# Performance work log

Hardware: AMD Instinct MI355X
Metric: run time of the kernel (lower is better)

Reference implementation:

```python
import jax, jax.numpy as jnp
import numpy as np

# irreps layout: 256x0e (dim 256) + 128x1o (dim 384) + 64x2e (dim 320) -> total 960
MULS = (256, 128, 64)
DIMS = (1, 3, 5)  # 2l+1 for l = 0, 1, 2


def setup_inputs() -> dict:
    key = jax.random.key(0)
    k0, k1, k2, k3 = jax.random.split(key, 4)
    N = 131072
    total = sum(m * d for m, d in zip(MULS, DIMS))  # 960
    return {
        "features": jax.random.normal(k0, (N, total), dtype=jnp.float32),
        "w0": jax.random.normal(k1, (256, 256), dtype=jnp.float32),
        "w1": jax.random.normal(k2, (128, 128), dtype=jnp.float32),
        "w2": jax.random.normal(k3, (64, 64), dtype=jnp.float32),
    }


def _linear_irreps(features, weights):
    # Equivariant Linear == block-diagonal per-irrep matmul over the multiplicity
    # axis, broadcast over the (2l+1) m-components, scaled by 1/sqrt(mul_in)
    # (the net of e3nn's path_weight sqrt((2l+1)/mul_in) and the w3j 1/sqrt(2l+1)).
    outs = []
    off = 0
    for w, mul, d in zip(weights, MULS, DIMS):
        x = features[:, off:off + mul * d].reshape(-1, mul, d)  # [N, u, i]
        scale = 1.0 / np.sqrt(mul).astype(np.float32)
        y = jnp.einsum('zui,uw->zwi', x, w) * scale  # [N, w, i]
        outs.append(y.reshape(y.shape[0], mul * d))
        off += mul * d
    return jnp.concatenate(outs, axis=-1)  # [N, 960]


def reference(features, w0, w1, w2):
    return _linear_irreps(features, (w0, w1, w2))
```

## Files before the change

kernel.cpp:

```cpp
#include <hip/hip_runtime.h>
#include <hip/hip_bf16.h>

typedef short bf16x8 __attribute__((ext_vector_type(8)));
typedef float f32x4 __attribute__((ext_vector_type(4)));
typedef unsigned short u16t;

__device__ __forceinline__ u16t f2bf(float f) {
    return __builtin_bit_cast(u16t, __float2bfloat16(f));
}

__device__ __forceinline__ f32x4 mfma16(bf16x8 a, bf16x8 b, f32x4 c) {
    return __builtin_amdgcn_mfma_f32_16x16x32_bf16(a, b, c, 0, 0, 0);
}

template<int D, int MUL>
__global__ void expand_w(const float* __restrict__ w, u16t* __restrict__ wt, float scale) {
    const int n = blockIdx.x;
    const int k = threadIdx.x;
    float v = 0.0f;
    if (D == 1 || (n % D) == (k % D))
        v = w[(k / D) * MUL + (n / D)] * scale;
    wt[n * (MUL * D) + k] = f2bf(v);
}

template<int KP, int NTH>
__device__ __forceinline__ void compute_half(const char* __restrict__ arow,
                                             const u16t* __restrict__ wb,
                                             float* __restrict__ orow,
                                             int nt0, int lr, int q) {
    constexpr int KS = KP / 32;
    f32x4 acc[4][NTH] = {};
    #pragma unroll
    for (int ks = 0; ks < KS; ++ks) {
        bf16x8 b[NTH];
        #pragma unroll
        for (int nt = 0; nt < NTH; ++nt)
            b[nt] = *(const bf16x8*)(wb + ((nt0 + nt) * 16 + lr) * KP + ks * 32 + q * 8);
        #pragma unroll
        for (int mt = 0; mt < 4; ++mt) {
            bf16x8 a = *(const bf16x8*)(arow + mt * 16 * KP * 2 +
                                        ((ks * 64 + q * 16) ^ ((lr & 7) << 4)));
            #pragma unroll
            for (int nt = 0; nt < NTH; ++nt)
                acc[mt][nt] = mfma16(a, b[nt], acc[mt][nt]);
        }
    }
    #pragma unroll
    for (int mt = 0; mt < 4; ++mt)
        #pragma unroll
        for (int nt = 0; nt < NTH; ++nt)
            #pragma unroll
            for (int j = 0; j < 4; ++j)
                orow[(mt * 16 + q * 4 + j) * 960 + (nt0 + nt) * 16 + lr] = acc[mt][nt][j];
}

template<int KP, int OFF, int NTH0, int NTH1>
__device__ __forceinline__ void do_block(const float* __restrict__ x,
                                         const u16t* __restrict__ wb,
                                         float* __restrict__ out,
                                         char* smem, long tile, int tid) {
    constexpr int C8  = KP / 8;
    constexpr int NCH = 64 * C8 / 256;
    constexpr int NTW = NTH0 + NTH1;
    const int lane = tid & 63, wv = tid >> 6, lr = lane & 15, q = lane >> 4;
    const float* xr = x + tile * 64 * 960 + OFF;
    float* orow = out + tile * 64 * 960 + OFF;

    #pragma unroll
    for (int it = 0; it < NCH; ++it) {
        int idx = tid + it * 256;
        int row = idx / C8;
        int c8  = idx % C8;
        const float* p = xr + row * 960 + c8 * 8;
        f32x4 v0 = *(const f32x4*)p;
        f32x4 v1 = *(const f32x4*)(p + 4);
        bf16x8 sv;
        sv[0] = f2bf(v0[0]); sv[1] = f2bf(v0[1]); sv[2] = f2bf(v0[2]); sv[3] = f2bf(v0[3]);
        sv[4] = f2bf(v1[0]); sv[5] = f2bf(v1[1]); sv[6] = f2bf(v1[2]); sv[7] = f2bf(v1[3]);
        *(bf16x8*)(smem + row * (KP * 2) + ((c8 * 16) ^ ((row & 7) << 4))) = sv;
    }
    __syncthreads();

    const char* arow = smem + lr * (KP * 2);
    compute_half<KP, NTH0>(arow, wb, orow, wv * NTW,        lr, q);
    compute_half<KP, NTH1>(arow, wb, orow, wv * NTW + NTH0, lr, q);
}

__global__ __launch_bounds__(256, 3)
void fused_linear(const float* __restrict__ x, const u16t* __restrict__ wt,
                  float* __restrict__ out) {
    __shared__ __align__(16) char smem[64 * 384 * 2];
    const long gid  = blockIdx.x;
    const int  bt   = (int)(gid % 3);
    const long tile = gid / 3;
    const int  tid  = threadIdx.x;
    if (bt == 0)      do_block<256,   0, 2, 2>(x, wt,          out, smem, tile, tid);
    else if (bt == 1) do_block<384, 256, 3, 3>(x, wt +  65536, out, smem, tile, tid);
    else              do_block<320, 640, 3, 2>(x, wt + 212992, out, smem, tile, tid);
}

extern "C" void kernel_launch(void* const* d_in, const int* in_sizes, int n_in,
                              void* d_out, int out_size, void* d_ws, size_t ws_size,
                              hipStream_t stream) {
    const float* x  = (const float*)d_in[0];
    const float* w0 = (const float*)d_in[1];
    const float* w1 = (const float*)d_in[2];
    const float* w2 = (const float*)d_in[3];
    float* out = (float*)d_out;
    u16t* wt = (u16t*)d_ws;

    const int N     = in_sizes[0] / 960;
    const int tiles = N / 64;

    expand_w<1, 256><<<256, 256, 0, stream>>>(w0, wt,          0.0625f);
    expand_w<3, 128><<<384, 384, 0, stream>>>(w1, wt +  65536, 0.08838834764831845f);
    expand_w<5,  64><<<320, 320, 0, stream>>>(w2, wt + 212992, 0.125f);

    fused_linear<<<3 * tiles, 256, 0, stream>>>(x, wt, out);
}
```

Measured before the change: 338.4 us.

## Use persistent grid with register-prefetched 32-row tiles and smaller per-wave output tiles

Turns the fused kernel into a persistent grid-stride loop over 32-row tiles. While the current tile is computed, the next tile's fp32 activations are prefetched into registers, so global load latency can overlap with the MFMA work. The per-wave tiling changes to 16 rows by 2 n-tiles per chunk and halves LDS use, allowing higher occupancy (launch bounds 5). In exchange, A-fragment reuse across rows drops, B loads from global are repeated more often, and each block needs two barriers per iteration.

Result: slower. 746.5 us (+120.6%).

```diff
diff --git a/kernel.cpp b/kernel.cpp
--- a/kernel.cpp
+++ b/kernel.cpp
@@ -23,80 +23,93 @@
     wt[n * (MUL * D) + k] = f2bf(v);
 }
 
-template<int KP, int NTH>
-__device__ __forceinline__ void compute_half(const char* __restrict__ arow,
-                                             const u16t* __restrict__ wb,
-                                             float* __restrict__ orow,
-                                             int nt0, int lr, int q) {
-    constexpr int KS = KP / 32;
-    f32x4 acc[4][NTH] = {};
-    #pragma unroll
-    for (int ks = 0; ks < KS; ++ks) {
-        bf16x8 b[NTH];
-        #pragma unroll
-        for (int nt = 0; nt < NTH; ++nt)
-            b[nt] = *(const bf16x8*)(wb + ((nt0 + nt) * 16 + lr) * KP + ks * 32 + q * 8);
-        #pragma unroll
-        for (int mt = 0; mt < 4; ++mt) {
-            bf16x8 a = *(const bf16x8*)(arow + mt * 16 * KP * 2 +
-                                        ((ks * 64 + q * 16) ^ ((lr & 7) << 4)));
-            #pragma unroll
-            for (int nt = 0; nt < NTH; ++nt)
-                acc[mt][nt] = mfma16(a, b[nt], acc[mt][nt]);
-        }
-    }
-    #pragma unroll
-    for (int mt = 0; mt < 4; ++mt)
-        #pragma unroll
-        for (int nt = 0; nt < NTH; ++nt)
-            #pragma unroll
-            for (int j = 0; j < 4; ++j)
-                orow[(mt * 16 + q * 4 + j) * 960 + (nt0 + nt) * 16 + lr] = acc[mt][nt][j];
-}
-
-template<int KP, int OFF, int NTH0, int NTH1>
+template<int KP, int OFF>
 __device__ __forceinline__ void do_block(const float* __restrict__ x,
                                          const u16t* __restrict__ wb,
                                          float* __restrict__ out,
-                                         char* smem, long tile, int tid) {
-    constexpr int C8  = KP / 8;
-    constexpr int NCH = 64 * C8 / 256;
-    constexpr int NTW = NTH0 + NTH1;
+                                         char* smem, int tile0, int tstride,
+                                         int ntiles, int tid) {
+    constexpr int C8 = KP / 8;
+    constexpr int IT = C8 / 8;
+    constexpr int KS = KP / 32;
+    constexpr int NT = KP / 16;
+    constexpr int CH = NT / 4;
     const int lane = tid & 63, wv = tid >> 6, lr = lane & 15, q = lane >> 4;
-    const float* xr = x + tile * 64 * 960 + OFF;
-    float* orow = out + tile * 64 * 960 + OFF;
+    const int mg = wv >> 1, ng = wv & 1;
 
+    f32x4 g[IT * 2];
     #pragma unroll
-    for (int it = 0; it < NCH; ++it) {
+    for (int it = 0; it < IT; ++it) {
         int idx = tid + it * 256;
-        int row = idx / C8;
-        int c8  = idx % C8;
-        const float* p = xr + row * 960 + c8 * 8;
-        f32x4 v0 = *(const f32x4*)p;
-        f32x4 v1 = *(const f32x4*)(p + 4);
-        bf16x8 sv;
-        sv[0] = f2bf(v0[0]); sv[1] = f2bf(v0[1]); sv[2] = f2bf(v0[2]); sv[3] = f2bf(v0[3]);
-        sv[4] = f2bf(v1[0]); sv[5] = f2bf(v1[1]); sv[6] = f2bf(v1[2]); sv[7] = f2bf(v1[3]);
-        *(bf16x8*)(smem + row * (KP * 2) + ((c8 * 16) ^ ((row & 7) << 4))) = sv;
+        int row = idx / C8, c8 = idx % C8;
+        const float* p = x + ((long)tile0 * 32 + row) * 960 + OFF + c8 * 8;
+        g[2 * it]     = *(const f32x4*)p;
+        g[2 * it + 1] = *(const f32x4*)(p + 4);
     }
-    __syncthreads();
 
-    const char* arow = smem + lr * (KP * 2);
-    compute_half<KP, NTH0>(arow, wb, orow, wv * NTW,        lr, q);
-    compute_half<KP, NTH1>(arow, wb, orow, wv * NTW + NTH0, lr, q);
+    for (int t = tile0; t < ntiles; t += tstride) {
+        #pragma unroll
+        for (int it = 0; it < IT; ++it) {
+            int idx = tid + it * 256;
+            int row = idx / C8, c8 = idx % C8;
+            bf16x8 sv;
+            #pragma unroll
+            for (int e = 0; e < 4; ++e) {
+                sv[e]     = f2bf(g[2 * it][e]);
+                sv[e + 4] = f2bf(g[2 * it + 1][e]);
+            }
+            *(bf16x8*)(smem + row * (KP * 2) + ((c8 * 16) ^ ((row & 7) << 4))) = sv;
+        }
+        asm volatile("s_waitcnt lgkmcnt(0)" ::: "memory");
+        __builtin_amdgcn_s_barrier();
+
+        {
+            int tn = t + tstride; if (tn >= ntiles) tn = t;
+            #pragma unroll
+            for (int it = 0; it < IT; ++it) {
+                int idx = tid + it * 256;
+                int row = idx / C8, c8 = idx % C8;
+                const float* p = x + ((long)tn * 32 + row) * 960 + OFF + c8 * 8;
+                g[2 * it]     = *(const f32x4*)p;
+                g[2 * it + 1] = *(const f32x4*)(p + 4);
+            }
+        }
+
+        const char* ar = smem + (mg * 16 + lr) * (KP * 2);
+        #pragma unroll
+        for (int c = 0; c < CH; ++c) {
+            const int ntg = ng * (NT / 2) + c * 2;
+            f32x4 acc0 = {0.f, 0.f, 0.f, 0.f}, acc1 = {0.f, 0.f, 0.f, 0.f};
+            #pragma unroll
+            for (int ks = 0; ks < KS; ++ks) {
+                bf16x8 a  = *(const bf16x8*)(ar + ((ks * 64 + q * 16) ^ ((lr & 7) << 4)));
+                bf16x8 b0 = *(const bf16x8*)(wb + ((ntg + 0) * 16 + lr) * KP + ks * 32 + q * 8);
+                bf16x8 b1 = *(const bf16x8*)(wb + ((ntg + 1) * 16 + lr) * KP + ks * 32 + q * 8);
+                acc0 = mfma16(a, b0, acc0);
+                acc1 = mfma16(a, b1, acc1);
+            }
+            float* ow = out + ((long)t * 32 + mg * 16 + q * 4) * 960 + OFF + ntg * 16 + lr;
+            #pragma unroll
+            for (int j = 0; j < 4; ++j) {
+                ow[j * 960]      = acc0[j];
+                ow[j * 960 + 16] = acc1[j];
+            }
+        }
+        __builtin_amdgcn_s_barrier();
+    }
 }
 
-__global__ __launch_bounds__(256, 3)
+__global__ __launch_bounds__(256, 5)
 void fused_linear(const float* __restrict__ x, const u16t* __restrict__ wt,
-                  float* __restrict__ out) {
-    __shared__ __align__(16) char smem[64 * 384 * 2];
-    const long gid  = blockIdx.x;
-    const int  bt   = (int)(gid % 3);
-    const long tile = gid / 3;
-    const int  tid  = threadIdx.x;
-    if (bt == 0)      do_block<256,   0, 2, 2>(x, wt,          out, smem, tile, tid);
-    else if (bt == 1) do_block<384, 256, 3, 3>(x, wt +  65536, out, smem, tile, tid);
-    else              do_block<320, 640, 3, 2>(x, wt + 212992, out, smem, tile, tid);
+                  float* __restrict__ out, int ntiles) {
+    __shared__ __align__(16) char smem[32 * 384 * 2];
+    const int bt = (int)(blockIdx.x % 3);
+    const int t0 = (int)(blockIdx.x / 3);
+    const int ts = (int)(gridDim.x / 3);
+    const int tid = threadIdx.x;
+    if (bt == 0)      do_block<256,   0>(x, wt,          out, smem, t0, ts, ntiles, tid);
+    else if (bt == 1) do_block<384, 256>(x, wt +  65536, out, smem, t0, ts, ntiles, tid);
+    else              do_block<320, 640>(x, wt + 212992, out, smem, t0, ts, ntiles, tid);
 }
 
 extern "C" void kernel_launch(void* const* d_in, const int* in_sizes, int n_in,
@@ -109,12 +122,13 @@
     float* out = (float*)d_out;
     u16t* wt = (u16t*)d_ws;
 
-    const int N     = in_sizes[0] / 960;
-    const int tiles = N / 64;
+    const int N      = in_sizes[0] / 960;
+    const int ntiles = N / 32;
+    const int gs     = (ntiles < 2048 ? ntiles : 2048);
 
     expand_w<1, 256><<<256, 256, 0, stream>>>(w0, wt,          0.0625f);
     expand_w<3, 128><<<384, 384, 0, stream>>>(w1, wt +  65536, 0.08838834764831845f);
     expand_w<5,  64><<<320, 320, 0, stream>>>(w2, wt + 212992, 0.125f);
 
-    fused_linear<<<3 * tiles, 256, 0, stream>>>(x, wt, out);
+    fused_linear<<<3 * gs, 256, 0, stream>>>(x, wt, out, ntiles);
 }
```
